# Optimization experiments

Measured on AMD Instinct MI355X. Metric: run time of the kernel, lower is better.

Reference implementation:

```python
import jax, jax.numpy as jnp
import numpy as np

TEMP = 0.1
NEG = -1e30  # stands in for removing the diagonal via masked_select
EPS = 1e-12  # F.normalize eps


def _l2norm(x, axis):
    n = jnp.linalg.norm(x, axis=axis, keepdims=True)
    return x / jnp.maximum(n, EPS)


def setup_inputs() -> dict:
    key = jax.random.key(0)
    k = jax.random.split(key, 6)
    B, D = 8192, 128      # instance batch, embed dim
    Bp, P = 256, 256      # patch batch, patches per sample
    v1_ins = jax.random.normal(k[0], (B, D), jnp.float32)
    v2_ins = jax.random.normal(k[1], (B, D), jnp.float32)
    v1_patch = jax.random.normal(k[2], (Bp, D, P), jnp.float32)
    v2_patch = jax.random.normal(k[3], (Bp, D, P), jnp.float32)
    v1_counts = jax.random.randint(k[4], (Bp, P), 0, 50, dtype=jnp.int32)
    v2_counts = jax.random.randint(k[5], (Bp, P), 0, 50, dtype=jnp.int32)
    return {"v1_ins": v1_ins, "v2_ins": v2_ins,
            "v1_patch": v1_patch, "v2_patch": v2_patch,
            "v1_counts": v1_counts, "v2_counts": v2_counts}


def _instance_ce(v1, v2):
    B = v1.shape[0]
    embs = jnp.concatenate([_l2norm(v1, 1), _l2norm(v2, 1)], axis=0)  # [2B, D]
    logits = (embs @ embs.T) / TEMP                                    # [2B, 2B]
    N = 2 * B
    # masking the diagonal to -inf == masked_select removal; positive of row i
    # is column (i+B) mod 2B (matches labels after diagonal removal shift)
    logits = jnp.where(jnp.eye(N, dtype=bool), NEG, logits)
    labels = jnp.concatenate([jnp.arange(B) + B, jnp.arange(B)])
    logp = jax.nn.log_softmax(logits, axis=1)
    return -jnp.mean(logp[jnp.arange(N), labels])


def _patch_ce(v1, v2, c1, c2):
    Bp, D, P = v1.shape
    embs = jnp.concatenate([_l2norm(v1, 1), _l2norm(v2, 1)], axis=2)   # [Bp, D, 2P]
    logits = jnp.einsum('bdi,bdj->bij', embs, embs) / TEMP             # [Bp, 2P, 2P]
    N = 2 * P
    logits = jnp.where(jnp.eye(N, dtype=bool)[None], NEG, logits)
    labels = jnp.concatenate([jnp.arange(P) + P, jnp.arange(P)])       # [2P]
    valid = ~jnp.concatenate([c1 == 0, c2 == 0], axis=1)               # [Bp, 2P]
    logp = jax.nn.log_softmax(logits, axis=2)
    pos = logp[:, jnp.arange(N), labels]                               # [Bp, 2P]
    # ignore_index=-100 -> mean over non-ignored elements
    n_valid = jnp.sum(valid.astype(logits.dtype))
    return -jnp.sum(jnp.where(valid, pos, 0.0)) / n_valid


def reference(v1_ins, v2_ins, v1_patch, v2_patch, v1_counts, v2_counts):
    ins_ce = _instance_ce(v1_ins, v2_ins)
    patch_ce = _patch_ce(v1_patch, v2_patch, v1_counts, v2_counts)
    return ins_ce + patch_ce
```

## Files before the change

### kernel.cpp

```cpp
#include <hip/hip_runtime.h>
#include <math.h>

typedef __bf16 bf16_t;
typedef __bf16 bf16x8 __attribute__((ext_vector_type(8)));
typedef float f32x4 __attribute__((ext_vector_type(4)));
typedef float f32x2 __attribute__((ext_vector_type(2)));

#define B_INS 8192
#define N_INS 16384
#define D 128
#define BP 256
#define P 256
#define NP 512

#define C1_CONST 14.426950408889634f
#define SQRT_C1 3.798283f
#define LN2_CONST 0.69314718056f

#define WS_ACC 0
#define WS_POS 8
#define WS_PPOS (WS_POS + N_INS)
#define NPAIRI 8128
#define WS_CI (WS_PPOS + BP * NP)
#define WS_RI (WS_CI + NPAIRI * 256)
#define WS_CP (WS_RI + 1088 * 256)
#define WS_RP (WS_CP + BP * 6 * 256)
#define WS_END (WS_RP + 1024 * 256)
#define EMB_I_BYTE ((((WS_END) * 4 + 15) / 16) * 16)
#define EMB_P_BYTE (EMB_I_BYTE + N_INS * D * 2)


#define NB_NORMI 128
#define NB_NORMP 2048
#define NB_PREP (NB_NORMI + NB_NORMP + 1)
#define NB_INS 1088
#define NB_PATCHB 1024
#define NB_GRAM (NB_INS + NB_PATCHB)
#define NB_FIN (128 + 256)

__device__ __forceinline__ void load_lds16(const bf16_t* g, bf16_t* l) {
    __builtin_amdgcn_global_load_lds(
        (const __attribute__((address_space(1))) void*)g,
        (__attribute__((address_space(3))) void*)l, 16, 0, 0);
}

__device__ __forceinline__ void stage_panel(const bf16_t* __restrict__ src,
                                            bf16_t* dst, int w, int lane) {
    const bf16_t* g = src + w * 4096 + lane * 8;
    bf16_t* d = dst + w * 4096;
#pragma unroll
    for (int it = 0; it < 8; it++)
        load_lds16(g + it * 512, d + it * 512);
}

__device__ __forceinline__ void load_afrags(const bf16_t* __restrict__ abase,
                                            int rh, int tx, int q, bf16x8 af[4][4]) {
    const bf16_t* a = abase + ((rh * 64 + tx) << 3);
#pragma unroll
    for (int rt = 0; rt < 4; rt++)
#pragma unroll
        for (int ks = 0; ks < 4; ks++)
            af[rt][ks] = *(const bf16x8*)(a + (((ks << 2) + q) << 10) + (rt << 7));
}

__global__ __launch_bounds__(256) void prep_k(const float* __restrict__ v1i,
                                              const float* __restrict__ v2i,
                                              const float* __restrict__ v1p,
                                              const float* __restrict__ v2p,
                                              bf16_t* __restrict__ embI,
                                              bf16_t* __restrict__ embP,
                                              float* __restrict__ ws) {
    __shared__ float L[128][65];
    __shared__ float ps[4][64];
    __shared__ float invs[128];
    int bx = blockIdx.x;
    int t = threadIdx.x;
    if (bx < NB_NORMI) {
        int p = bx;
        const float* srcP = (p < 64) ? (v1i + (size_t)p * 128 * D)
                                     : (v2i + (size_t)(p - 64) * 128 * D);
        {
            int r = t >> 1, h = t & 1;
            const float* row = srcP + (size_t)r * D + h * 64;
            float ss = 0.f;
#pragma unroll
            for (int j = 0; j < 16; j++) {
                float4 v = *(const float4*)(row + j * 4);
                ss += v.x * v.x + v.y * v.y + v.z * v.z + v.w * v.w;
            }
            ss += __shfl_xor(ss, 1, 64);
            if (h == 0) invs[r] = SQRT_C1 / fmaxf(sqrtf(ss), 1e-12f);
        }
        __syncthreads();
#pragma unroll
        for (int it = 0; it < 8; it++) {
            int idx = it * 256 + t;
            int r = idx & 127, g = idx >> 7;
            const float* src8 = srcP + (size_t)r * D + g * 8;
            float4 a = *(const float4*)(src8);
            float4 b = *(const float4*)(src8 + 4);
            float inv = invs[r];
            bf16x8 v;
            v[0] = (bf16_t)(a.x * inv); v[1] = (bf16_t)(a.y * inv);
            v[2] = (bf16_t)(a.z * inv); v[3] = (bf16_t)(a.w * inv);
            v[4] = (bf16_t)(b.x * inv); v[5] = (bf16_t)(b.y * inv);
            v[6] = (bf16_t)(b.z * inv); v[7] = (bf16_t)(b.w * inv);
            *(bf16x8*)(embI + ((size_t)p << 14) + (g << 10) + (r << 3)) = v;
        }
    } else if (bx < NB_NORMI + NB_NORMP) {
        int bx2 = bx - NB_NORMI;
        int b = bx2 >> 3, h = (bx2 >> 2) & 1, chunk = bx2 & 3;
        int i0 = chunk * 64;
        const float* src = ((h == 0) ? v1p : v2p) + (size_t)b * D * P;
#pragma unroll
        for (int it = 0; it < 8; it++) {
            int fi = it * 256 + t;
            int d = fi >> 4, c4 = fi & 15;
            float4 v = *(const float4*)(src + (size_t)d * P + i0 + c4 * 4);
            L[d][c4 * 4 + 0] = v.x;
            L[d][c4 * 4 + 1] = v.y;
            L[d][c4 * 4 + 2] = v.z;
            L[d][c4 * 4 + 3] = v.w;
        }
        __syncthreads();
        {
            int col = t & 63, part = t >> 6;
            float ss = 0.f;
#pragma unroll 8
            for (int d = part * 32; d < part * 32 + 32; d++) { float x = L[d][col]; ss += x * x; }
            ps[part][col] = ss;
        }
        __syncthreads();
        if (t < 64) {
            float n2 = ps[0][t] + ps[1][t] + ps[2][t] + ps[3][t];
            invs[t] = SQRT_C1 / fmaxf(sqrtf(n2), 1e-12f);
        }
        __syncthreads();
#pragma unroll
        for (int it = 0; it < 4; it++) {
            int idx = it * 256 + t;
            int ic = idx & 63, g = idx >> 6;
            float inv = invs[ic];
            bf16x8 v;
#pragma unroll
            for (int j = 0; j < 8; j++) v[j] = (bf16_t)(L[g * 8 + j][ic] * inv);
            int iLoc = h * P + i0 + ic;
            *(bf16x8*)(embP + ((size_t)b << 16) + ((size_t)(iLoc >> 7) << 14) +
                       (g << 10) + ((iLoc & 127) << 3)) = v;
        }
    } else {
        if (t < 8) ws[t] = 0.f;
    }
}

__global__ __launch_bounds__(256) void gram_k(const bf16_t* __restrict__ embI,
                                              const bf16_t* __restrict__ embP,
                                              float* __restrict__ pos,
                                              float* __restrict__ posp,
                                              float* __restrict__ colI,
                                              float* __restrict__ rowI,
                                              float* __restrict__ colP,
                                              float* __restrict__ rowP) {
    __shared__ __align__(16) bf16_t shB[2][16384];
    int t = threadIdx.x, w = t >> 6, lane = t & 63;
    int tx = lane & 15, q = lane >> 4;
    int rh = w & 1, ch = w >> 1;
    int bx = blockIdx.x;

    const bf16_t *Abase, *Bbase;
    float *posArr, *colArr, *rowDst;
    int R, c0, n, diagC, posC;
    if (bx < NB_INS) {
        int bid = bx, k = 0, cum = 0;
        while (bid >= cum + 8 * (16 - k)) { cum += 8 * (16 - k); k++; }
        int rem = bid - cum, cc = 16 - k;
        R = 8 * k + rem / cc;
        int ci = rem - (rem / cc) * cc;
        c0 = R + ci * 8;
        n = min(8, 128 - c0);
        Abase = embI + ((size_t)R << 14);
        Bbase = embI;
        posArr = pos;
        colArr = colI + (size_t)R * 256;
        rowDst = rowI + (size_t)(R * 16 + ci) * 256;
        diagC = R; posC = R + 64;
    } else {
        int pi = bx - NB_INS;
        int b = pi >> 2; R = pi & 3;
        c0 = R; n = 4 - R;
        const bf16_t* base = embP + ((size_t)b << 16);
        Abase = base + ((size_t)R << 14);
        Bbase = base;
        posArr = posp + (size_t)b * NP;
        colArr = colP + (size_t)(b * 6 + R) * 256;
        rowDst = rowP + (size_t)((b << 2) + R) * 256;
        diagC = R; posC = R + 2;
    }
    int rowBase = R * 128;

    bf16x8 af[4][4];
    load_afrags(Abase, rh, tx, q, af);

    f32x2 rowS2[8];
#pragma unroll
    for (int i = 0; i < 8; i++) rowS2[i] = (f32x2){0.f, 0.f};

#define LOADBF(BF, NT)                                                        \
    _Pragma("unroll") for (int ks = 0; ks < 4; ks++)                          \
        BF[ks] = *(const bf16x8*)(sb + (((ks << 2) + q) << 10) +              \
                                  ((ch * 64 + (NT) * 16 + tx) << 3));

#define MFMAS(ACC, BF)                                                        \
    _Pragma("unroll") for (int rt = 0; rt < 4; rt++)                          \
        ACC[rt] = (f32x4){-C1_CONST, -C1_CONST, -C1_CONST, -C1_CONST};        \
    __builtin_amdgcn_s_setprio(1);                                            \
    _Pragma("unroll") for (int ks = 0; ks < 4; ks++)                          \
        _Pragma("unroll") for (int rt = 0; rt < 4; rt++)                      \
            ACC[rt] = __builtin_amdgcn_mfma_f32_16x16x32_bf16(                \
                af[rt][ks], BF[ks], ACC[rt], 0, 0, 0);                        \
    __builtin_amdgcn_s_setprio(0);

#define EPI(NT, ACC) {                                                        \
    f32x2 cs = (f32x2){0.f, 0.f};                                             \
    _Pragma("unroll") for (int rt = 0; rt < 4; rt++) {                        \
        f32x2 e0 = {__builtin_amdgcn_exp2f(ACC[rt][0]),                       \
                    __builtin_amdgcn_exp2f(ACC[rt][1])};                      \
        f32x2 e1 = {__builtin_amdgcn_exp2f(ACC[rt][2]),                       \
                    __builtin_amdgcn_exp2f(ACC[rt][3])};                      \
        if (isDiag) {                                                         \
            int inRow = rh * 64 + rt * 16 + q * 4;                            \
            int inCol = ch * 64 + (NT) * 16 + tx;                             \
            if (inRow + 0 == inCol) e0.x = 0.f;                               \
            if (inRow + 1 == inCol) e0.y = 0.f;                               \
            if (inRow + 2 == inCol) e1.x = 0.f;                               \
            if (inRow + 3 == inCol) e1.y = 0.f;                               \
        }                                                                     \
        rowS2[rt * 2] += e0;                                                  \
        rowS2[rt * 2 + 1] += e1;                                              \
        cs += e0 + e1;                                                        \
    }                                                                         \
    colS[NT] = cs.x + cs.y;                                                   \
    if (isPos && ch == rh) {                                                  \
        int reg = tx - q * 4;                                                 \
        if (reg >= 0 && reg < 4) {                                            \
            float pl = (ACC[NT][reg] + C1_CONST) * LN2_CONST;                 \
            posArr[rowBase + rh * 64 + (NT) * 16 + tx] = pl;                  \
            posArr[colBase + rh * 64 + (NT) * 16 + tx] = pl;                  \
        }                                                                     \
    } }

    stage_panel(Bbase + ((size_t)c0 << 14), shB[0], w, lane);
    int cur = 0;
    for (int ti = 0; ti < n; ti++) {
        int C = c0 + ti;
        __syncthreads();
        if (ti + 1 < n)
            stage_panel(Bbase + ((size_t)(C + 1) << 14), shB[cur ^ 1], w, lane);
        bool isDiag = (C == diagC), isPos = (C == posC);
        int colBase = C * 128;
        const bf16_t* sb = shB[cur];

        float colS[4];
        bf16x8 bfA[4], bfB[4];
        f32x4 accA[4], accB[4];
        LOADBF(bfA, 0) MFMAS(accA, bfA)
        LOADBF(bfB, 1) MFMAS(accB, bfB)
        EPI(0, accA)
        LOADBF(bfA, 2) MFMAS(accA, bfA)
        EPI(1, accB)
        LOADBF(bfB, 3) MFMAS(accB, bfB)
        EPI(2, accA)
        EPI(3, accB)

        if (!isDiag) {
#pragma unroll
            for (int i = 0; i < 4; i++) {
                colS[i] += __shfl_xor(colS[i], 16, 64);
                colS[i] += __shfl_xor(colS[i], 32, 64);
            }
            if (q == 0) {
                float* cdst = colArr + (size_t)(C * (C - 1) / 2) * 256 + rh * 128;
#pragma unroll
                for (int nt = 0; nt < 4; nt++)
                    cdst[ch * 64 + nt * 16 + tx] = colS[nt];
            }
        }
        cur ^= 1;
    }
    float* rowS = (float*)rowS2;
#pragma unroll
    for (int off = 1; off <= 8; off <<= 1)
#pragma unroll
        for (int i = 0; i < 16; i++) rowS[i] += __shfl_xor(rowS[i], off, 16);
    if (tx == 0) {
#pragma unroll
        for (int rt = 0; rt < 4; rt++)
#pragma unroll
            for (int reg = 0; reg < 4; reg++)
                rowDst[ch * 128 + rh * 64 + rt * 16 + q * 4 + reg] =
                    rowS[rt * 4 + reg];
    }
#undef LOADBF
#undef MFMAS
#undef EPI
}

__global__ __launch_bounds__(512) void fin_k(const float* __restrict__ pos,
                                             const float* __restrict__ posp,
                                             const float* __restrict__ colI,
                                             const float* __restrict__ rowI,
                                             const float* __restrict__ colP,
                                             const float* __restrict__ rowP,
                                             const int* __restrict__ c1,
                                             const int* __restrict__ c2,
                                             float* __restrict__ acc,
                                             float* __restrict__ out) {
    int bx = blockIdx.x, t = threadIdx.x;
    int lane = t & 63, w = t >> 6;
    float va = 0.f, nv = 0.f;
    __shared__ float part[2][2][128];
    if (bx < 128) {
        int p = 127 - bx;
        int u = t >> 8, half = (t >> 7) & 1, r = t & 127;
        int cc = 16 - (p >> 3);
        float s0 = 0.f, s1 = 0.f, s2 = 0.f, s3 = 0.f;
        const float* RIp = rowI + (size_t)(p * 16) * 256 + half * 128 + r;
        int ci = u;
        for (; ci + 6 < cc; ci += 8) {
            s0 += RIp[ci * 256];       s1 += RIp[(ci + 2) * 256];
            s2 += RIp[(ci + 4) * 256]; s3 += RIp[(ci + 6) * 256];
        }
        for (; ci < cc; ci += 2) s0 += RIp[ci * 256];
        const float* CIp = colI + (size_t)(p * (p - 1) / 2) * 256 + half * 128 + r;
        int Rq = u;
        for (; Rq + 6 < p; Rq += 8) {
            s0 += CIp[Rq * 256];       s1 += CIp[(Rq + 2) * 256];
            s2 += CIp[(Rq + 4) * 256]; s3 += CIp[(Rq + 6) * 256];
        }
        for (; Rq < p; Rq += 2) s0 += CIp[Rq * 256];
        part[u][half][r] = (s0 + s1) + (s2 + s3);
        __syncthreads();
        if (t < 128) {
            float S = (part[0][0][t] + part[0][1][t]) +
                      (part[1][0][t] + part[1][1][t]);
            va = __logf(S) + 10.0f - pos[p * 128 + t];
        }
    } else {
        int b = bx - 128;
        int idx = t;
        int p = idx >> 7, r = idx & 127;
        const float* RPp = rowP + (size_t)((b << 2) + p) * 256 + r;
        float s = RPp[0] + RPp[128];
        const float* CPp = colP + (size_t)(b * 6 + p * (p - 1) / 2) * 256 + r;
        for (int Rq = 0; Rq < p; Rq++) s += CPp[Rq * 256] + CPp[Rq * 256 + 128];
        int cnt = (idx < P) ? c1[b * P + idx] : c2[b * P + idx - P];
        if (cnt != 0) {
            va = __logf(s) + 10.0f - posp[b * NP + idx];
            nv = 1.0f;
        }
    }
#pragma unroll
    for (int off = 32; off >= 1; off >>= 1) {
        va += __shfl_down(va, off, 64);
        nv += __shfl_down(nv, off, 64);
    }
    __shared__ float psum[8], pn[8];
    if (lane == 0) { psum[w] = va; pn[w] = nv; }
    __syncthreads();
    if (t == 0) {
        float sv = 0.f, sn = 0.f;
#pragma unroll
        for (int i = 0; i < 8; i++) { sv += psum[i]; sn += pn[i]; }
        if (bx < 128) {
            atomicAdd(&acc[0], sv);
        } else {
            atomicAdd(&acc[1], sv);
            atomicAdd(&acc[2], sn);
        }
        __threadfence();
        unsigned old = atomicAdd((unsigned*)&acc[3], 1u);
        if (old == NB_FIN - 1) {
            float a0 = atomicAdd(&acc[0], 0.0f);
            float a1 = atomicAdd(&acc[1], 0.0f);
            float a2 = atomicAdd(&acc[2], 0.0f);
            out[0] = a0 * (1.0f / (float)N_INS) + a1 / a2;
        }
    }
}

extern "C" void kernel_launch(void* const* d_in, const int* in_sizes, int n_in,
                              void* d_out, int out_size, void* d_ws, size_t ws_size,
                              hipStream_t stream) {
    const float* v1i = (const float*)d_in[0];
    const float* v2i = (const float*)d_in[1];
    const float* v1p = (const float*)d_in[2];
    const float* v2p = (const float*)d_in[3];
    const int* c1 = (const int*)d_in[4];
    const int* c2 = (const int*)d_in[5];
    float* ws = (float*)d_ws;
    float* out = (float*)d_out;
    bf16_t* embI = (bf16_t*)((char*)d_ws + EMB_I_BYTE);
    bf16_t* embP = (bf16_t*)((char*)d_ws + EMB_P_BYTE);

    prep_k<<<NB_PREP, 256, 0, stream>>>(v1i, v2i, v1p, v2p, embI, embP, ws);
    gram_k<<<NB_GRAM, 256, 0, stream>>>(embI, embP, ws + WS_POS, ws + WS_PPOS,
                                        ws + WS_CI, ws + WS_RI,
                                        ws + WS_CP, ws + WS_RP);
    fin_k<<<NB_FIN, 512, 0, stream>>>(ws + WS_POS, ws + WS_PPOS, ws + WS_CI,
                                      ws + WS_RI, ws + WS_CP, ws + WS_RP,
                                      c1, c2, ws + WS_ACC, out);
}
```

Measured before the change: 203.3 us.

## Share staged B panels between two row-panels per 512-thread gram block

Each gram block now runs 8 waves and handles two adjacent row panels (R and R+1), which share the same double-buffered LDS column panels. Each wave group skips columns below its own row. This halves the global-to-LDS staging traffic per computed tile and halves the block count. In exchange, one wave group sits idle on the first column, the blocks are larger, and the row-partial indexing in the final kernel changes to match.

New measurement: 207.8 us. +2.3%, slower.

```diff
diff --git a/kernel.cpp b/kernel.cpp
--- a/kernel.cpp
+++ b/kernel.cpp
@@ -23,7 +23,7 @@
 #define NPAIRI 8128
 #define WS_CI (WS_PPOS + BP * NP)
 #define WS_RI (WS_CI + NPAIRI * 256)
-#define WS_CP (WS_RI + 1088 * 256)
+#define WS_CP (WS_RI + 2048 * 256)
 #define WS_RP (WS_CP + BP * 6 * 256)
 #define WS_END (WS_RP + 1024 * 256)
 #define EMB_I_BYTE ((((WS_END) * 4 + 15) / 16) * 16)
@@ -33,9 +33,9 @@
 #define NB_NORMI 128
 #define NB_NORMP 2048
 #define NB_PREP (NB_NORMI + NB_NORMP + 1)
-#define NB_INS 1088
-#define NB_PATCHB 1024
-#define NB_GRAM (NB_INS + NB_PATCHB)
+#define NB_INSP 544
+#define NB_PATCHP 512
+#define NB_GRAMP (NB_INSP + NB_PATCHP)
 #define NB_FIN (128 + 256)
 
 __device__ __forceinline__ void load_lds16(const bf16_t* g, bf16_t* l) {
@@ -44,12 +44,12 @@
         (__attribute__((address_space(3))) void*)l, 16, 0, 0);
 }
 
-__device__ __forceinline__ void stage_panel(const bf16_t* __restrict__ src,
-                                            bf16_t* dst, int w, int lane) {
-    const bf16_t* g = src + w * 4096 + lane * 8;
-    bf16_t* d = dst + w * 4096;
-#pragma unroll
-    for (int it = 0; it < 8; it++)
+__device__ __forceinline__ void stage_panel8(const bf16_t* __restrict__ src,
+                                             bf16_t* dst, int w, int lane) {
+    const bf16_t* g = src + w * 2048 + lane * 8;
+    bf16_t* d = dst + w * 2048;
+#pragma unroll
+    for (int it = 0; it < 4; it++)
         load_lds16(g + it * 512, d + it * 512);
 }
 
@@ -153,7 +153,7 @@
     }
 }
 
-__global__ __launch_bounds__(256) void gram_k(const bf16_t* __restrict__ embI,
+__global__ __launch_bounds__(512) void gram_k(const bf16_t* __restrict__ embI,
                                               const bf16_t* __restrict__ embP,
                                               float* __restrict__ pos,
                                               float* __restrict__ posp,
@@ -164,19 +164,19 @@
     __shared__ __align__(16) bf16_t shB[2][16384];
     int t = threadIdx.x, w = t >> 6, lane = t & 63;
     int tx = lane & 15, q = lane >> 4;
-    int rh = w & 1, ch = w >> 1;
+    int pn = w >> 2, ch = (w >> 1) & 1, rh = w & 1;
     int bx = blockIdx.x;
 
     const bf16_t *Abase, *Bbase;
     float *posArr, *colArr, *rowDst;
     int R, c0, n, diagC, posC;
-    if (bx < NB_INS) {
-        int bid = bx, k = 0, cum = 0;
-        while (bid >= cum + 8 * (16 - k)) { cum += 8 * (16 - k); k++; }
-        int rem = bid - cum, cc = 16 - k;
-        R = 8 * k + rem / cc;
-        int ci = rem - (rem / cc) * cc;
-        c0 = R + ci * 8;
+    if (bx < NB_INSP) {
+        int bid = bx, k = 0, cum = 0, cc2 = 16;
+        while (bid >= cum + cc2) { cum += cc2; k++; cc2 = (135 - 2 * k) >> 3; }
+        int ci = bid - cum;
+        int Ra = 2 * k;
+        R = Ra + pn;
+        c0 = Ra + ci * 8;
         n = min(8, 128 - c0);
         Abase = embI + ((size_t)R << 14);
         Bbase = embI;
@@ -185,9 +185,11 @@
         rowDst = rowI + (size_t)(R * 16 + ci) * 256;
         diagC = R; posC = R + 64;
     } else {
-        int pi = bx - NB_INS;
-        int b = pi >> 2; R = pi & 3;
-        c0 = R; n = 4 - R;
+        int pi = bx - NB_INSP;
+        int b = pi >> 1, p2 = pi & 1;
+        int Ra = 2 * p2;
+        R = Ra + pn;
+        c0 = Ra; n = 4 - Ra;
         const bf16_t* base = embP + ((size_t)b << 16);
         Abase = base + ((size_t)R << 14);
         Bbase = base;
@@ -249,40 +251,42 @@
         }                                                                     \
     } }
 
-    stage_panel(Bbase + ((size_t)c0 << 14), shB[0], w, lane);
+    stage_panel8(Bbase + ((size_t)c0 << 14), shB[0], w, lane);
     int cur = 0;
     for (int ti = 0; ti < n; ti++) {
         int C = c0 + ti;
         __syncthreads();
         if (ti + 1 < n)
-            stage_panel(Bbase + ((size_t)(C + 1) << 14), shB[cur ^ 1], w, lane);
-        bool isDiag = (C == diagC), isPos = (C == posC);
-        int colBase = C * 128;
-        const bf16_t* sb = shB[cur];
-
-        float colS[4];
-        bf16x8 bfA[4], bfB[4];
-        f32x4 accA[4], accB[4];
-        LOADBF(bfA, 0) MFMAS(accA, bfA)
-        LOADBF(bfB, 1) MFMAS(accB, bfB)
-        EPI(0, accA)
-        LOADBF(bfA, 2) MFMAS(accA, bfA)
-        EPI(1, accB)
-        LOADBF(bfB, 3) MFMAS(accB, bfB)
-        EPI(2, accA)
-        EPI(3, accB)
-
-        if (!isDiag) {
-#pragma unroll
-            for (int i = 0; i < 4; i++) {
-                colS[i] += __shfl_xor(colS[i], 16, 64);
-                colS[i] += __shfl_xor(colS[i], 32, 64);
-            }
-            if (q == 0) {
-                float* cdst = colArr + (size_t)(C * (C - 1) / 2) * 256 + rh * 128;
-#pragma unroll
-                for (int nt = 0; nt < 4; nt++)
-                    cdst[ch * 64 + nt * 16 + tx] = colS[nt];
+            stage_panel8(Bbase + ((size_t)(C + 1) << 14), shB[cur ^ 1], w, lane);
+        if (C >= R) {
+            bool isDiag = (C == diagC), isPos = (C == posC);
+            int colBase = C * 128;
+            const bf16_t* sb = shB[cur];
+
+            float colS[4];
+            bf16x8 bfA[4], bfB[4];
+            f32x4 accA[4], accB[4];
+            LOADBF(bfA, 0) MFMAS(accA, bfA)
+            LOADBF(bfB, 1) MFMAS(accB, bfB)
+            EPI(0, accA)
+            LOADBF(bfA, 2) MFMAS(accA, bfA)
+            EPI(1, accB)
+            LOADBF(bfB, 3) MFMAS(accB, bfB)
+            EPI(2, accA)
+            EPI(3, accB)
+
+            if (!isDiag) {
+#pragma unroll
+                for (int i = 0; i < 4; i++) {
+                    colS[i] += __shfl_xor(colS[i], 16, 64);
+                    colS[i] += __shfl_xor(colS[i], 32, 64);
+                }
+                if (q == 0) {
+                    float* cdst = colArr + (size_t)(C * (C - 1) / 2) * 256 + rh * 128;
+#pragma unroll
+                    for (int nt = 0; nt < 4; nt++)
+                        cdst[ch * 64 + nt * 16 + tx] = colS[nt];
+                }
             }
         }
         cur ^= 1;
@@ -322,7 +326,7 @@
     if (bx < 128) {
         int p = 127 - bx;
         int u = t >> 8, half = (t >> 7) & 1, r = t & 127;
-        int cc = 16 - (p >> 3);
+        int cc = (135 - (p & 126)) >> 3;
         float s0 = 0.f, s1 = 0.f, s2 = 0.f, s3 = 0.f;
         const float* RIp = rowI + (size_t)(p * 16) * 256 + half * 128 + r;
         int ci = u;
@@ -403,9 +407,9 @@
     bf16_t* embP = (bf16_t*)((char*)d_ws + EMB_P_BYTE);
 
     prep_k<<<NB_PREP, 256, 0, stream>>>(v1i, v2i, v1p, v2p, embI, embP, ws);
-    gram_k<<<NB_GRAM, 256, 0, stream>>>(embI, embP, ws + WS_POS, ws + WS_PPOS,
-                                        ws + WS_CI, ws + WS_RI,
-                                        ws + WS_CP, ws + WS_RP);
+    gram_k<<<NB_GRAMP, 512, 0, stream>>>(embI, embP, ws + WS_POS, ws + WS_PPOS,
+                                         ws + WS_CI, ws + WS_RI,
+                                         ws + WS_CP, ws + WS_RP);
     fin_k<<<NB_FIN, 512, 0, stream>>>(ws + WS_POS, ws + WS_PPOS, ws + WS_CI,
                                       ws + WS_RI, ws + WS_CP, ws + WS_RP,
                                       c1, c2, ws + WS_ACC, out);
```
